# Kernel tuning notes

Measured on AMD Instinct MI355X. Metric: run time of the kernel, lower is better.

Reference implementation:

```python
import jax, jax.numpy as jnp
import numpy as np
import math

B, T, NC = 16, 256, 2
_NS = (9, 9, 11, 11, 9, 20)  # legacy6 region node counts
_OUT, _RF, _FD, _NH, _FF = 32, 64, 128, 4, 2048


def _region_adj(n):
    # chain + second-order edges (legacy6), plus self-loops; GCN sym-normalized
    A = np.zeros((n, n), np.float32)
    for i in range(n - 1):
        A[i, i + 1] = A[i + 1, i] = 1.0
    for i in range(n - 2):
        A[i, i + 2] = A[i + 2, i] = 1.0
    A = A + np.eye(n, dtype=np.float32)
    d = A.sum(1) ** -0.5
    return jnp.asarray(d[:, None] * A * d[None, :])

_ADJS = [_region_adj(n) for n in _NS]


def _pe_table(t, d):
    pos = np.arange(t, dtype=np.float32)[:, None]
    div = np.exp(np.arange(0, d, 2, dtype=np.float32) * (-math.log(10000.0) / d))
    pe = np.zeros((t, d), np.float32)
    pe[:, 0::2] = np.sin(pos * div)
    pe[:, 1::2] = np.cos(pos * div)
    return jnp.asarray(pe)

_PE = _pe_table(T, _FD)


def _ln(x, g, b, eps=1e-5):
    m = jnp.mean(x, -1, keepdims=True)
    v = jnp.mean((x - m) ** 2, -1, keepdims=True)
    return (x - m) / jnp.sqrt(v + eps) * g + b


def _mha(q, kv, qkv_w, qkv_b, ow, ob, nh):
    d = q.shape[-1]
    hd = d // nh
    wq, wk, wv = jnp.split(qkv_w, 3, axis=1)
    bq, bk, bv = jnp.split(qkv_b, 3)
    def sp(x):
        return x.reshape(x.shape[0], x.shape[1], nh, hd).transpose(0, 2, 1, 3)
    Q, K, V = sp(q @ wq + bq), sp(kv @ wk + bk), sp(kv @ wv + bv)
    att = jax.nn.softmax(jnp.einsum('bhqd,bhkd->bhqk', Q, K) / jnp.sqrt(jnp.float32(hd)), axis=-1)
    o = jnp.einsum('bhqk,bhkd->bhqd', att, V).transpose(0, 2, 1, 3).reshape(q.shape[0], q.shape[1], d)
    return o @ ow + ob


def _tel(x, qkv_w, qkv_b, ow, ob, l1g, l1b, f1w, f1b, f2w, f2b, l2g, l2b, nh):
    # torch post-norm TransformerEncoderLayer (relu FFN, eval mode: no dropout)
    x = _ln(x + _mha(x, x, qkv_w, qkv_b, ow, ob, nh), l1g, l1b)
    ff = jax.nn.relu(x @ f1w + f1b) @ f2w + f2b
    return _ln(x + ff, l2g, l2b)


def setup_inputs() -> dict:
    key = jax.random.key(0)
    ks = iter(jax.random.split(key, 80))
    def nrm(shape, s=0.05):
        return jax.random.normal(next(ks), shape, jnp.float32) * s
    inp = {}
    for name, n in zip(('x_ljaw', 'x_rjaw', 'x_leye', 'x_reye', 'x_nose', 'x_mouth'), _NS):
        inp[name] = jax.random.normal(next(ks), (B, T, n, 11), jnp.float32)
    inp['global_feats'] = jax.random.normal(next(ks), (B, T, 4), jnp.float32)
    inp['global_alpha'] = jnp.float32(0.2)
    inp['gcn1_w'] = nrm((6, 11, _OUT)); inp['gcn1_b'] = jnp.zeros((6, _OUT))
    inp['gcn2_w'] = nrm((6, _OUT, _OUT)); inp['gcn2_b'] = jnp.zeros((6, _OUT))
    inp['rln_g'] = jnp.ones((6, _RF)); inp['rln_b'] = jnp.zeros((6, _RF))
    inp['sp_qkv_w'] = nrm((_RF, 3 * _RF)); inp['sp_qkv_b'] = jnp.zeros((3 * _RF,))
    inp['sp_out_w'] = nrm((_RF, _RF)); inp['sp_out_b'] = jnp.zeros((_RF,))
    inp['sp_ln1_g'] = jnp.ones((_RF,)); inp['sp_ln1_b'] = jnp.zeros((_RF,))
    inp['sp_ff1_w'] = nrm((_RF, _FF)); inp['sp_ff1_b'] = jnp.zeros((_FF,))
    inp['sp_ff2_w'] = nrm((_FF, _RF)); inp['sp_ff2_b'] = jnp.zeros((_RF,))
    inp['sp_ln2_g'] = jnp.ones((_RF,)); inp['sp_ln2_b'] = jnp.zeros((_RF,))
    priors = np.array([0.3, 0.3, 0.8, 0.8, 0.4, 1.0], np.float32)
    inp['region_logits'] = jnp.asarray(np.log(np.expm1(priors)).reshape(1, 6, 1))
    inp['gate1_w'] = nrm((_RF, 32)); inp['gate1_b'] = jnp.zeros((32,))
    inp['gate2_w'] = nrm((32, 1)); inp['gate2_b'] = jnp.zeros((1,))
    inp['ca_qkv_w'] = nrm((_RF, 3 * _RF)); inp['ca_qkv_b'] = jnp.zeros((3 * _RF,))
    inp['ca_out_w'] = nrm((_RF, _RF)); inp['ca_out_b'] = jnp.zeros((_RF,))
    inp['ca_ln_g'] = jnp.ones((_RF,)); inp['ca_ln_b'] = jnp.zeros((_RF,))
    inp['glob_w'] = nrm((4, _RF)); inp['glob_b'] = jnp.zeros((_RF,))
    inp['glob_ln_g'] = jnp.ones((_RF,)); inp['glob_ln_b'] = jnp.zeros((_RF,))
    inp['fused_ln_g'] = jnp.ones((_FD,)); inp['fused_ln_b'] = jnp.zeros((_FD,))
    inp['tp_qkv_w'] = nrm((_FD, 3 * _FD)); inp['tp_qkv_b'] = jnp.zeros((3 * _FD,))
    inp['tp_out_w'] = nrm((_FD, _FD)); inp['tp_out_b'] = jnp.zeros((_FD,))
    inp['tp_ln1_g'] = jnp.ones((_FD,)); inp['tp_ln1_b'] = jnp.zeros((_FD,))
    inp['tp_ff1_w'] = nrm((_FD, _FF)); inp['tp_ff1_b'] = jnp.zeros((_FF,))
    inp['tp_ff2_w'] = nrm((_FF, _FD)); inp['tp_ff2_b'] = jnp.zeros((_FD,))
    inp['tp_ln2_g'] = jnp.ones((_FD,)); inp['tp_ln2_b'] = jnp.zeros((_FD,))
    inp['attnproj_w'] = nrm((_FD, 1)); inp['attnproj_b'] = jnp.zeros((1,))
    inp['cls1_w'] = nrm((_FD, _OUT)); inp['cls1_b'] = jnp.zeros((_OUT,))
    inp['cls_ln_g'] = jnp.ones((_OUT,)); inp['cls_ln_b'] = jnp.zeros((_OUT,))
    inp['cls2_w'] = nrm((_OUT, NC)); inp['cls2_b'] = jnp.zeros((NC,))
    return inp


def reference(x_ljaw, x_rjaw, x_leye, x_reye, x_nose, x_mouth, global_feats, global_alpha, gcn1_w, gcn1_b, gcn2_w, gcn2_b, rln_g, rln_b, sp_qkv_w, sp_qkv_b, sp_out_w, sp_out_b, sp_ln1_g, sp_ln1_b, sp_ff1_w, sp_ff1_b, sp_ff2_w, sp_ff2_b, sp_ln2_g, sp_ln2_b, region_logits, gate1_w, gate1_b, gate2_w, gate2_b, ca_qkv_w, ca_qkv_b, ca_out_w, ca_out_b, ca_ln_g, ca_ln_b, glob_w, glob_b, glob_ln_g, glob_ln_b, fused_ln_g, fused_ln_b, tp_qkv_w, tp_qkv_b, tp_out_w, tp_out_b, tp_ln1_g, tp_ln1_b, tp_ff1_w, tp_ff1_b, tp_ff2_w, tp_ff2_b, tp_ln2_g, tp_ln2_b, attnproj_w, attnproj_b, cls1_w, cls1_b, cls_ln_g, cls_ln_b, cls2_w, cls2_b):
    xs = (x_ljaw, x_rjaw, x_leye, x_reye, x_nose, x_mouth)
    Bc, Tc = x_ljaw.shape[0], x_ljaw.shape[1]
    # per-region 2-layer GCN + concat(mean,max) node pooling -> (B,T,64) tokens
    toks = []
    for i in range(6):
        A = _ADJS[i]
        h = jax.nn.relu(jnp.einsum('nm,btmf->btnf', A, xs[i] @ gcn1_w[i]) + gcn1_b[i])
        h = jax.nn.relu(jnp.einsum('nm,btmf->btnf', A, h @ gcn2_w[i]) + gcn2_b[i])
        feat = jnp.concatenate([h.mean(2), h.max(2)], -1)
        toks.append(_ln(feat, rln_g[i], rln_b[i]))
    tok = jnp.stack(toks, 2).reshape(Bc * Tc, 6, _RF)
    # spatial transformer over the 6 region tokens per frame
    tok = _tel(tok, sp_qkv_w, sp_qkv_b, sp_out_w, sp_out_b, sp_ln1_g, sp_ln1_b, sp_ff1_w, sp_ff1_b, sp_ff2_w, sp_ff2_b, sp_ln2_g, sp_ln2_b, _NH)
    # learned region priors (softplus) * per-sample sigmoid gates
    rw = jax.nn.softplus(region_logits)
    gate = jax.nn.sigmoid(jax.nn.relu(tok @ gate1_w + gate1_b) @ gate2_w + gate2_b)
    tok = tok * rw * gate
    # cross-attn fusion: mean-region query attends over region tokens
    q = jnp.mean(tok, 1, keepdims=True)
    attn = _mha(q, tok, ca_qkv_w, ca_qkv_b, ca_out_w, ca_out_b, _NH)
    fused_r = _ln(q[:, 0] + attn[:, 0], ca_ln_g, ca_ln_b)
    # gated global branch (4 -> 64), concat to fused_dim=128
    g = jax.nn.relu(_ln(global_feats.reshape(Bc * Tc, 4) @ glob_w + glob_b, glob_ln_g, glob_ln_b))
    g = jnp.tanh(global_alpha) * g
    fused = _ln(jnp.concatenate([fused_r, g], -1), fused_ln_g, fused_ln_b).reshape(Bc, Tc, _FD)
    # temporal transformer + attention pooling over time
    fused = fused + _PE[None, :Tc]
    h = _tel(fused, tp_qkv_w, tp_qkv_b, tp_out_w, tp_out_b, tp_ln1_g, tp_ln1_b, tp_ff1_w, tp_ff1_b, tp_ff2_w, tp_ff2_b, tp_ln2_g, tp_ln2_b, _NH)
    wt = jax.nn.softmax(h @ attnproj_w + attnproj_b, axis=1)
    pooled = jnp.sum(wt * h, 1)
    z = jax.nn.relu(_ln(pooled @ cls1_w + cls1_b, cls_ln_g, cls_ln_b))
    return z @ cls2_w + cls2_b
```

## Files before the change

kernel.cpp:

```cpp
#include <hip/hip_runtime.h>
#include <math.h>
#include <stddef.h>

#define NFRM 4096
#define NBATCH 16

typedef __attribute__((ext_vector_type(8))) short short8v;
typedef __attribute__((ext_vector_type(4))) float f32x4;
#define MFMA_BF16(a,b,c) __builtin_amdgcn_mfma_f32_16x16x32_bf16(a,b,c,0,0,0)

__device__ inline float wsum64(float v){
  #pragma unroll
  for(int m=32;m>=1;m>>=1) v += __shfl_xor(v, m, 64);
  return v;
}

__device__ inline float pe_val(int t,int d){
  int k = d >> 1;
  float div = expf(-(float)(2*k) * (9.210340371976184f/128.f));
  float ang = (float)t * div;
  return (d & 1) ? cosf(ang) : sinf(ang);
}

__device__ inline void bf16split(float x, unsigned short &h, unsigned short &l){
  unsigned u = __float_as_uint(x);
  unsigned r = (u + 0x7FFFu + ((u>>16)&1u)) & 0xFFFF0000u;
  h = (unsigned short)(r>>16);
  float rem = x - __uint_as_float(r);
  unsigned u2 = __float_as_uint(rem);
  unsigned r2 = (u2 + 0x7FFFu + ((u2>>16)&1u));
  l = (unsigned short)(r2>>16);
}

__global__ __launch_bounds__(64) void pack_w_kernel(
    const float* __restrict__ w, unsigned short* __restrict__ hi,
    unsigned short* __restrict__ lo, int K, int N)
{
  int ntile = blockIdx.x, s = blockIdx.y, lane = threadIdx.x;
  int n = ntile*16 + (lane & 15);
  int k0 = s*32 + (lane>>4)*8;
  size_t off = (((size_t)ntile*(K/32) + s)*64 + lane)*8;
  #pragma unroll
  for(int e=0;e<8;e++){
    float v = w[(size_t)(k0+e)*N + n];
    unsigned short h,l;
    bf16split(v,h,l);
    hi[off+e]=h; lo[off+e]=l;
  }
}

template<int D, int NS>
__global__ __launch_bounds__(256) void ffn_mfma_partial(
    const float* __restrict__ X, float* __restrict__ P,
    const unsigned short* __restrict__ w1h, const unsigned short* __restrict__ w1l,
    const float* __restrict__ b1,
    const unsigned short* __restrict__ w2h, const unsigned short* __restrict__ w2l)
{
  constexpr int TM=32, JC=128;
  constexpr int KS1 = D/32;
  constexpr int NT2W = (D/16)/4;
  constexpr int HS = 2048/NS;
  constexpr int NCH = HS/JC;
  constexpr int HP = JC + 8;
  __shared__ unsigned short Hh[TM][HP];
  __shared__ unsigned short Hl[TM][HP];
  int tid = threadIdx.x;
  int lane = tid & 63, w = tid >> 6;
  int ar = lane & 15, ak = lane >> 4;
  size_t Ntok = (size_t)gridDim.x*TM;
  const float* Xb = X + (size_t)blockIdx.x*TM*D;

  short8v xah[2][KS1], xal[2][KS1];
  #pragma unroll
  for(int mt=0;mt<2;mt++){
    #pragma unroll
    for(int s=0;s<KS1;s++){
      const float* xp = Xb + (size_t)(mt*16+ar)*D + s*32 + ak*8;
      #pragma unroll
      for(int e=0;e<8;e++){
        unsigned short h,l;
        bf16split(xp[e],h,l);
        xah[mt][s][e]=(short)h; xal[mt][s][e]=(short)l;
      }
    }
  }

  f32x4 acc2[2][NT2W];
  #pragma unroll
  for(int mt=0;mt<2;mt++)
    #pragma unroll
    for(int nt=0;nt<NT2W;nt++)
      acc2[mt][nt] = (f32x4){0.f,0.f,0.f,0.f};

  for(int ch=0; ch<NCH; ch++){
    int jc = blockIdx.y*HS + ch*JC;
    f32x4 a1[2][2];
    #pragma unroll
    for(int mt=0;mt<2;mt++){ a1[mt][0]=(f32x4){0,0,0,0}; a1[mt][1]=(f32x4){0,0,0,0}; }
    #pragma unroll
    for(int s=0;s<KS1;s++){
      #pragma unroll
      for(int nt=0;nt<2;nt++){
        int ntile1 = (jc + w*32 + nt*16) >> 4;
        size_t off = (((size_t)ntile1*KS1 + s)*64 + lane)*8;
        short8v bh = *(const short8v*)(w1h + off);
        short8v bl = *(const short8v*)(w1l + off);
        #pragma unroll
        for(int mt=0;mt<2;mt++){
          a1[mt][nt] = MFMA_BF16(xah[mt][s], bh, a1[mt][nt]);
          a1[mt][nt] = MFMA_BF16(xah[mt][s], bl, a1[mt][nt]);
          a1[mt][nt] = MFMA_BF16(xal[mt][s], bh, a1[mt][nt]);
        }
      }
    }
    __syncthreads();
    #pragma unroll
    for(int nt=0;nt<2;nt++){
      int colBase = w*32 + nt*16 + ar;
      float bval = b1[jc + colBase];
      #pragma unroll
      for(int mt=0;mt<2;mt++){
        #pragma unroll
        for(int r=0;r<4;r++){
          float hv = a1[mt][nt][r] + bval;
          hv = fmaxf(hv, 0.f);
          unsigned short h,l;
          bf16split(hv,h,l);
          int row = mt*16 + ak*4 + r;
          Hh[row][colBase]=h; Hl[row][colBase]=l;
        }
      }
    }
    __syncthreads();
    #pragma unroll
    for(int s2=0;s2<4;s2++){
      short8v ah[2], al[2];
      #pragma unroll
      for(int mt=0;mt<2;mt++){
        ah[mt] = *(const short8v*)&Hh[mt*16+ar][s2*32 + ak*8];
        al[mt] = *(const short8v*)&Hl[mt*16+ar][s2*32 + ak*8];
      }
      #pragma unroll
      for(int nt=0;nt<NT2W;nt++){
        int ntile2 = w*NT2W + nt;
        int kstep2 = (jc >> 5) + s2;
        size_t off = (((size_t)ntile2*64 + kstep2)*64 + lane)*8;
        short8v bh = *(const short8v*)(w2h + off);
        short8v bl = *(const short8v*)(w2l + off);
        #pragma unroll
        for(int mt=0;mt<2;mt++){
          acc2[mt][nt] = MFMA_BF16(ah[mt], bh, acc2[mt][nt]);
          acc2[mt][nt] = MFMA_BF16(ah[mt], bl, acc2[mt][nt]);
          acc2[mt][nt] = MFMA_BF16(al[mt], bh, acc2[mt][nt]);
        }
      }
    }
  }
  float* Pb = P + (size_t)blockIdx.y*Ntok*D + (size_t)blockIdx.x*TM*D;
  #pragma unroll
  for(int mt=0;mt<2;mt++){
    #pragma unroll
    for(int nt=0;nt<NT2W;nt++){
      int col = (w*NT2W + nt)*16 + ar;
      #pragma unroll
      for(int r=0;r<4;r++){
        int row = mt*16 + ak*4 + r;
        Pb[(size_t)row*D + col] = acc2[mt][nt][r];
      }
    }
  }
}

template<int D, int NS>
__global__ __launch_bounds__(256) void ffn_combine_kernel(
    const float* __restrict__ X, const float* __restrict__ P,
    float* __restrict__ Y,
    const float* __restrict__ b2,
    const float* __restrict__ lg, const float* __restrict__ lb)
{
  constexpr int EPL = D/64;
  int tid=threadIdx.x;
  int lane = tid & 63;
  size_t Ntok = (size_t)gridDim.x*4;
  size_t row = (size_t)blockIdx.x*4 + (tid>>6);
  size_t base = row*D;
  float e[EPL];
  float s=0.f;
  #pragma unroll
  for(int i=0;i<EPL;i++){
    int c = i*64+lane;
    float v = X[base+c] + b2[c];
    #pragma unroll
    for(int sp=0;sp<NS;sp++) v += P[(size_t)sp*Ntok*D + base + c];
    e[i]=v; s+=v;
  }
  float mm = wsum64(s)*(1.f/D);
  float s2=0.f;
  #pragma unroll
  for(int i=0;i<EPL;i++){ float d=e[i]-mm; s2+=d*d; }
  float rs = rsqrtf(wsum64(s2)*(1.f/D)+1e-5f);
  #pragma unroll
  for(int i=0;i<EPL;i++){
    int c=i*64+lane;
    Y[base+c] = (e[i]-mm)*rs*lg[c]+lb[c];
  }
}

__global__ __launch_bounds__(256) void gcn_kernel(
    const float* __restrict__ x0,const float* __restrict__ x1,
    const float* __restrict__ x2,const float* __restrict__ x3,
    const float* __restrict__ x4,const float* __restrict__ x5,
    const float* __restrict__ g1w,const float* __restrict__ g1b,
    const float* __restrict__ g2w,const float* __restrict__ g2b,
    const float* __restrict__ rg,const float* __restrict__ rb,
    float* __restrict__ tok)
{
  int tid=threadIdx.x;
  int lane = tid & 63, w = tid >> 6;
  int f = blockIdx.x*4 + w;
  int r = blockIdx.y;
  int n = (r==5) ? 20 : ((r==2 || r==3) ? 11 : 9);
  const float* xr = (r==0)?x0:(r==1)?x1:(r==2)?x2:(r==3)?x3:(r==4)?x4:x5;

  __shared__ float xs[4][220];
  __shared__ float t0g[4][768];
  __shared__ float t1[4][640];
  __shared__ float C[20][5];
  __shared__ float W1s[11*32];
  __shared__ float W2s[32*32];
  __shared__ float b1s[32], b2s[32];

  for(int i=tid;i<4*768;i+=256) ((float*)t0g)[i]=0.f;
  for(int i=tid;i<352;i+=256) W1s[i]=g1w[r*11*32+i];
  for(int i=tid;i<1024;i+=256) W2s[i]=g2w[r*32*32+i];
  if(tid<32){ b1s[tid]=g1b[r*32+tid]; b2s[tid]=g2b[r*32+tid]; }
  if(tid<100){
    int node=tid/5, j=tid%5, m=node+j-2;
    float cf=0.f;
    if(node<n && m>=0 && m<n){
      int di = 1 + min(node,2) + min(n-1-node,2);
      int dm = 1 + min(m,2) + min(n-1-m,2);
      cf = rsqrtf((float)(di*dm));
    }
    C[node][j]=cf;
  }
  for(int i=lane;i<n*11;i+=64) xs[w][i] = xr[(size_t)f*n*11 + i];
  __syncthreads();
  for(int i=lane;i<n*32;i+=64){
    int node=i>>5, c=i&31;
    float s=0.f;
    #pragma unroll
    for(int k=0;k<11;k++) s += xs[w][node*11+k]*W1s[k*32+c];
    t0g[w][(node+2)*32+c]=s;
  }
  __syncthreads();
  for(int i=lane;i<n*32;i+=64){
    int node=i>>5, c=i&31;
    float s=b1s[c];
    #pragma unroll
    for(int j=0;j<5;j++) s += C[node][j]*t0g[w][(node+j)*32+c];
    t1[w][i]=fmaxf(s,0.f);
  }
  __syncthreads();
  for(int i=lane;i<n*32;i+=64){
    int node=i>>5, c=i&31;
    float s=0.f;
    #pragma unroll
    for(int k=0;k<32;k++) s += t1[w][node*32+k]*W2s[k*32+c];
    t0g[w][(node+2)*32+c]=s;
  }
  __syncthreads();
  for(int i=lane;i<n*32;i+=64){
    int node=i>>5, c=i&31;
    float s=b2s[c];
    #pragma unroll
    for(int j=0;j<5;j++) s += C[node][j]*t0g[w][(node+j)*32+c];
    t1[w][i]=fmaxf(s,0.f);
  }
  __syncthreads();
  float v;
  if(lane<32){
    float s=0.f;
    for(int m=0;m<n;m++) s += t1[w][m*32+lane];
    v = s/(float)n;
  } else {
    int c=lane-32;
    float mx=-1e30f;
    for(int m=0;m<n;m++) mx = fmaxf(mx, t1[w][m*32+c]);
    v = mx;
  }
  float m1 = wsum64(v)*(1.f/64.f);
  float d1 = v - m1;
  float var = wsum64(d1*d1)*(1.f/64.f);
  float y = d1*rsqrtf(var+1e-5f)*rg[r*64+lane] + rb[r*64+lane];
  tok[((size_t)f*6+r)*64+lane] = y;
}

__global__ __launch_bounds__(256) void sp_attn_kernel(
    float* __restrict__ tok,
    const float* __restrict__ qkvw,const float* __restrict__ qkvb,
    const float* __restrict__ ow,const float* __restrict__ ob,
    const float* __restrict__ l1g,const float* __restrict__ l1b)
{
  __shared__ float Xs[24][64];
  __shared__ float QKV[24][192];
  __shared__ float SC[4][144];
  __shared__ float AO[24][64];
  int tid=threadIdx.x;
  int f0 = blockIdx.x*4;
  float* Xf = &Xs[0][0];
  for(int i=tid;i<1536;i+=256) Xf[i] = tok[(size_t)f0*384 + i];
  __syncthreads();
  {
    int cg = tid & 31, c0 = cg*6;
    int rg = tid >> 5, r0 = rg*3;
    float acc[3][6];
    #pragma unroll
    for(int m=0;m<3;m++)
      #pragma unroll
      for(int j=0;j<6;j++) acc[m][j]=qkvb[c0+j];
    for(int k=0;k<64;k++){
      float wv[6];
      #pragma unroll
      for(int j=0;j<6;j++) wv[j]=qkvw[k*192+c0+j];
      float xv0=Xs[r0][k], xv1=Xs[r0+1][k], xv2=Xs[r0+2][k];
      #pragma unroll
      for(int j=0;j<6;j++){
        acc[0][j]+=xv0*wv[j];
        acc[1][j]+=xv1*wv[j];
        acc[2][j]+=xv2*wv[j];
      }
    }
    #pragma unroll
    for(int m=0;m<3;m++)
      #pragma unroll
      for(int j=0;j<6;j++) QKV[r0+m][c0+j]=acc[m][j];
  }
  __syncthreads();
  for(int i=tid;i<576;i+=256){
    int fr=i/144, rest=i%144;
    int h=rest/36, qi=(rest%36)/6, ki=rest%6;
    float s=0.f;
    #pragma unroll
    for(int d=0;d<16;d++) s += QKV[fr*6+qi][h*16+d]*QKV[fr*6+ki][64+h*16+d];
    SC[fr][rest]=s*0.25f;
  }
  __syncthreads();
  if(tid<96){
    int fr=tid/24, idx=tid%24;
    int base=idx*6;
    float mx=-1e30f;
    for(int k=0;k<6;k++) mx=fmaxf(mx,SC[fr][base+k]);
    float sm=0.f;
    for(int k=0;k<6;k++){ float e=expf(SC[fr][base+k]-mx); SC[fr][base+k]=e; sm+=e; }
    float rr=1.f/sm;
    for(int k=0;k<6;k++) SC[fr][base+k]*=rr;
  }
  __syncthreads();
  for(int i=tid;i<1536;i+=256){
    int fr=i/384, rem=i%384;
    int row=rem/64, c=rem&63, h=c/16;
    float s=0.f;
    #pragma unroll
    for(int k=0;k<6;k++) s += SC[fr][h*36+row*6+k]*QKV[fr*6+k][128+c];
    AO[fr*6+row][c]=s;
  }
  __syncthreads();
  {
    int cg = tid & 31, c0 = cg*2;
    int rg = tid >> 5, r0 = rg*3;
    float acc[3][2];
    #pragma unroll
    for(int m=0;m<3;m++){ acc[m][0]=ob[c0]; acc[m][1]=ob[c0+1]; }
    for(int k=0;k<64;k++){
      float w0=ow[k*64+c0], w1=ow[k*64+c0+1];
      float a0=AO[r0][k], a1=AO[r0+1][k], a2=AO[r0+2][k];
      acc[0][0]+=a0*w0; acc[0][1]+=a0*w1;
      acc[1][0]+=a1*w0; acc[1][1]+=a1*w1;
      acc[2][0]+=a2*w0; acc[2][1]+=a2*w1;
    }
    #pragma unroll
    for(int m=0;m<3;m++){
      QKV[r0+m][c0]   = Xs[r0+m][c0]   + acc[m][0];
      QKV[r0+m][c0+1] = Xs[r0+m][c0+1] + acc[m][1];
    }
  }
  __syncthreads();
  {
    int lane = tid & 63, w = tid >> 6;
    #pragma unroll
    for(int rr=0;rr<6;rr++){
      int row = w*6+rr;
      float v=QKV[row][lane];
      float mm=wsum64(v)*(1.f/64.f);
      float d=v-mm;
      float var=wsum64(d*d)*(1.f/64.f);
      tok[(size_t)f0*384 + row*64 + lane]=d*rsqrtf(var+1e-5f)*l1g[lane]+l1b[lane];
    }
  }
}

template<int D, int TM>
__global__ __launch_bounds__(256) void ffn_ln_kernel(
    const float* __restrict__ X, float* __restrict__ Yout,
    const float* __restrict__ w1,const float* __restrict__ b1,
    const float* __restrict__ w2,const float* __restrict__ b2,
    const float* __restrict__ lg,const float* __restrict__ lb)
{
  constexpr int JC = 128;
  constexpr int JS = JC + 4;
  constexpr int M1 = TM/8;
  constexpr int CG = D/4;
  constexpr int MG2 = 256/CG;
  constexpr int M2 = TM/MG2;
  __shared__ float Xs[TM*D];
  __shared__ float Hs[TM*JS];
  int tid=threadIdx.x;
  const float* Xb = X + (size_t)blockIdx.x*TM*D;
  for(int i=tid;i<TM*D;i+=256) Xs[i]=Xb[i];

  int jg = tid & 31, j0 = jg*4;
  int mg1 = tid >> 5;
  int m10 = mg1*M1;
  int cg = tid % CG, c0 = cg*4;
  int mg2 = tid / CG;
  int m20 = mg2*M2;

  float acc[M2][4];
  #pragma unroll
  for(int m=0;m<M2;m++){ acc[m][0]=0.f;acc[m][1]=0.f;acc[m][2]=0.f;acc[m][3]=0.f; }

  __syncthreads();
  for(int jc=0;jc<2048;jc+=JC){
    float a1[M1][4];
    float4 bv = *(const float4*)&b1[jc+j0];
    #pragma unroll
    for(int m=0;m<M1;m++){ a1[m][0]=bv.x;a1[m][1]=bv.y;a1[m][2]=bv.z;a1[m][3]=bv.w; }
    for(int k0=0;k0<D;k0+=4){
      float4 wr0 = *(const float4*)&w1[(size_t)(k0+0)*2048 + jc + j0];
      float4 wr1 = *(const float4*)&w1[(size_t)(k0+1)*2048 + jc + j0];
      float4 wr2 = *(const float4*)&w1[(size_t)(k0+2)*2048 + jc + j0];
      float4 wr3 = *(const float4*)&w1[(size_t)(k0+3)*2048 + jc + j0];
      #pragma unroll
      for(int m=0;m<M1;m++){
        float4 xv = *(const float4*)&Xs[(m10+m)*D + k0];
        a1[m][0] += xv.x*wr0.x + xv.y*wr1.x + xv.z*wr2.x + xv.w*wr3.x;
        a1[m][1] += xv.x*wr0.y + xv.y*wr1.y + xv.z*wr2.y + xv.w*wr3.y;
        a1[m][2] += xv.x*wr0.z + xv.y*wr1.z + xv.z*wr2.z + xv.w*wr3.z;
        a1[m][3] += xv.x*wr0.w + xv.y*wr1.w + xv.z*wr2.w + xv.w*wr3.w;
      }
    }
    #pragma unroll
    for(int m=0;m<M1;m++){
      float4 hv;
      hv.x=fmaxf(a1[m][0],0.f); hv.y=fmaxf(a1[m][1],0.f);
      hv.z=fmaxf(a1[m][2],0.f); hv.w=fmaxf(a1[m][3],0.f);
      *(float4*)&Hs[(m10+m)*JS + j0] = hv;
    }
    __syncthreads();
    for(int jj0=0;jj0<JC;jj0+=4){
      float4 w20 = *(const float4*)&w2[(size_t)(jc+jj0+0)*D + c0];
      float4 w21 = *(const float4*)&w2[(size_t)(jc+jj0+1)*D + c0];
      float4 w22 = *(const float4*)&w2[(size_t)(jc+jj0+2)*D + c0];
      float4 w23 = *(const float4*)&w2[(size_t)(jc+jj0+3)*D + c0];
      #pragma unroll
      for(int m=0;m<M2;m++){
        float4 hv = *(const float4*)&Hs[(m20+m)*JS + jj0];
        acc[m][0] += hv.x*w20.x + hv.y*w21.x + hv.z*w22.x + hv.w*w23.x;
        acc[m][1] += hv.x*w20.y + hv.y*w21.y + hv.z*w22.y + hv.w*w23.y;
        acc[m][2] += hv.x*w20.z + hv.y*w21.z + hv.z*w22.z + hv.w*w23.z;
        acc[m][3] += hv.x*w20.w + hv.y*w21.w + hv.z*w22.w + hv.w*w23.w;
      }
    }
    __syncthreads();
  }
  {
    float4 b2v = *(const float4*)&b2[c0];
    #pragma unroll
    for(int m=0;m<M2;m++){
      int row = m20+m;
      float4 xv = *(const float4*)&Xs[row*D + c0];
      float4 yv;
      yv.x = xv.x + acc[m][0] + b2v.x;
      yv.y = xv.y + acc[m][1] + b2v.y;
      yv.z = xv.z + acc[m][2] + b2v.z;
      yv.w = xv.w + acc[m][3] + b2v.w;
      *(float4*)&Hs[row*D + c0] = yv;
    }
  }
  __syncthreads();
  constexpr int EPL = D/64;
  int lane = tid & 63, wv = tid >> 6;
  float* Yb = Yout + (size_t)blockIdx.x*TM*D;
  for(int row=wv; row<TM; row+=4){
    float e[EPL];
    float s=0.f;
    #pragma unroll
    for(int i=0;i<EPL;i++){ e[i]=Hs[row*D + i*64 + lane]; s+=e[i]; }
    float mm = wsum64(s)*(1.f/D);
    float s2=0.f;
    #pragma unroll
    for(int i=0;i<EPL;i++){ float d=e[i]-mm; s2+=d*d; }
    float rs = rsqrtf(wsum64(s2)*(1.f/D)+1e-5f);
    #pragma unroll
    for(int i=0;i<EPL;i++)
      Yb[row*D + i*64 + lane] = (e[i]-mm)*rs*lg[i*64+lane]+lb[i*64+lane];
  }
}

__global__ __launch_bounds__(256) void fuse_kernel(
    const float* __restrict__ tok, const float* __restrict__ gfeat,
    const float* __restrict__ alpha_p, const float* __restrict__ rlogit,
    const float* __restrict__ g1w,const float* __restrict__ g1b,
    const float* __restrict__ g2w,const float* __restrict__ g2b,
    const float* __restrict__ caqw,const float* __restrict__ caqb,
    const float* __restrict__ caow,const float* __restrict__ caob,
    const float* __restrict__ calng,const float* __restrict__ calnb,
    const float* __restrict__ gw,const float* __restrict__ gb,
    const float* __restrict__ glng,const float* __restrict__ glnb,
    const float* __restrict__ flng,const float* __restrict__ flnb,
    float* __restrict__ fused)
{
  int tid=threadIdx.x;
  int lane = tid & 63, w = tid >> 6;
  int f = blockIdx.x*4 + w;
  __shared__ float X[4][384];
  __shared__ float G1[4][192];
  __shared__ float gt[4][6];
  __shared__ float qv[4][64];
  __shared__ float Qs[4][64];
  __shared__ float KK[4][384], VV[4][384];
  __shared__ float sc[4][24];
  __shared__ float AOs[4][64];

  const float* trow = tok + (size_t)f*384;
  for(int i=lane;i<384;i+=64) X[w][i]=trow[i];
  __syncthreads();
  for(int i=lane;i<192;i+=64){
    int rr=i/32, j=i%32;
    float s=g1b[j];
    #pragma unroll
    for(int k=0;k<64;k++) s += X[w][rr*64+k]*g1w[k*32+j];
    G1[w][i]=fmaxf(s,0.f);
  }
  __syncthreads();
  if(lane<6){
    float s=g2b[0];
    #pragma unroll
    for(int k=0;k<32;k++) s += G1[w][lane*32+k]*g2w[k];
    float gate = 1.f/(1.f+expf(-s));
    float rw = log1pf(expf(rlogit[lane]));
    gt[w][lane]=gate*rw;
  }
  __syncthreads();
  for(int i=lane;i<384;i+=64) X[w][i]*=gt[w][i/64];
  __syncthreads();
  {
    float s=0.f;
    #pragma unroll
    for(int rr=0;rr<6;rr++) s+=X[w][rr*64+lane];
    qv[w][lane]=s*(1.f/6.f);
  }
  __syncthreads();
  {
    float s=caqb[lane];
    #pragma unroll
    for(int k=0;k<64;k++) s += qv[w][k]*caqw[k*192+lane];
    Qs[w][lane]=s;
  }
  for(int i=lane;i<384;i+=64){
    int rr=i/64, c=i%64;
    float sk=caqb[64+c], sv=caqb[128+c];
    #pragma unroll
    for(int k=0;k<64;k++){
      float xv=X[w][rr*64+k];
      sk += xv*caqw[k*192+64+c];
      sv += xv*caqw[k*192+128+c];
    }
    KK[w][i]=sk; VV[w][i]=sv;
  }
  __syncthreads();
  if(lane<24){
    int h=lane/6, ki=lane%6;
    float s=0.f;
    #pragma unroll
    for(int d=0;d<16;d++) s += Qs[w][h*16+d]*KK[w][ki*64+h*16+d];
    sc[w][lane]=s*0.25f;
  }
  __syncthreads();
  if(lane<4){
    float mx=-1e30f;
    for(int k=0;k<6;k++) mx=fmaxf(mx,sc[w][lane*6+k]);
    float sm=0.f;
    for(int k=0;k<6;k++){ float e=expf(sc[w][lane*6+k]-mx); sc[w][lane*6+k]=e; sm+=e; }
    float rr=1.f/sm;
    for(int k=0;k<6;k++) sc[w][lane*6+k]*=rr;
  }
  __syncthreads();
  {
    int h=lane/16;
    float s=0.f;
    #pragma unroll
    for(int k=0;k<6;k++) s += sc[w][h*6+k]*VV[w][k*64+lane];
    AOs[w][lane]=s;
  }
  __syncthreads();
  float pr;
  {
    float s=caob[lane];
    #pragma unroll
    for(int k=0;k<64;k++) s += AOs[w][k]*caow[k*64+lane];
    pr = qv[w][lane] + s;
  }
  float m1=wsum64(pr)*(1.f/64.f);
  float d1=pr-m1;
  float v1=wsum64(d1*d1)*(1.f/64.f);
  float fr = d1*rsqrtf(v1+1e-5f)*calng[lane]+calnb[lane];
  float gvv;
  {
    float s=gb[lane];
    #pragma unroll
    for(int k=0;k<4;k++) s += gfeat[(size_t)f*4+k]*gw[k*64+lane];
    gvv=s;
  }
  float m2=wsum64(gvv)*(1.f/64.f);
  float d2=gvv-m2;
  float v2=wsum64(d2*d2)*(1.f/64.f);
  float gg = fmaxf(d2*rsqrtf(v2+1e-5f)*glng[lane]+glnb[lane],0.f)*tanhf(alpha_p[0]);
  float sm_ = wsum64(fr+gg)*(1.f/128.f);
  float da=fr-sm_, db=gg-sm_;
  float vv = wsum64(da*da+db*db)*(1.f/128.f);
  float rs = rsqrtf(vv+1e-5f);
  int t = f & 255;
  fused[(size_t)f*128+lane]     = da*rs*flng[lane]+flnb[lane]         + pe_val(t,lane);
  fused[(size_t)f*128+64+lane]  = db*rs*flng[64+lane]+flnb[64+lane]   + pe_val(t,64+lane);
}

__global__ __launch_bounds__(256) void tqkv_gemm_kernel(
    const float* __restrict__ X, float* __restrict__ Y,
    const float* __restrict__ w, const float* __restrict__ b)
{
  __shared__ float Xs[32*128];
  int tid=threadIdx.x;
  const float* Xb = X + (size_t)blockIdx.x*32*128;
  for(int i=tid;i<4096;i+=256) Xs[i]=Xb[i];
  __syncthreads();
  int cg = tid & 31, c0 = cg*4;
  int mg = tid >> 5, m0 = mg*4;
  float* Yb = Y + (size_t)blockIdx.x*32*384;
  int oc = blockIdx.y*128;
  float acc[4][4];
  float4 bv = *(const float4*)&b[oc+c0];
  #pragma unroll
  for(int m=0;m<4;m++){ acc[m][0]=bv.x;acc[m][1]=bv.y;acc[m][2]=bv.z;acc[m][3]=bv.w; }
  for(int k0=0;k0<128;k0+=4){
    float4 w0 = *(const float4*)&w[(k0+0)*384 + oc + c0];
    float4 w1 = *(const float4*)&w[(k0+1)*384 + oc + c0];
    float4 w2 = *(const float4*)&w[(k0+2)*384 + oc + c0];
    float4 w3 = *(const float4*)&w[(k0+3)*384 + oc + c0];
    #pragma unroll
    for(int m=0;m<4;m++){
      float4 xv = *(const float4*)&Xs[(m0+m)*128 + k0];
      acc[m][0] += xv.x*w0.x + xv.y*w1.x + xv.z*w2.x + xv.w*w3.x;
      acc[m][1] += xv.x*w0.y + xv.y*w1.y + xv.z*w2.y + xv.w*w3.y;
      acc[m][2] += xv.x*w0.z + xv.y*w1.z + xv.z*w2.z + xv.w*w3.z;
      acc[m][3] += xv.x*w0.w + xv.y*w1.w + xv.z*w2.w + xv.w*w3.w;
    }
  }
  #pragma unroll
  for(int m=0;m<4;m++){
    float4 yv; yv.x=acc[m][0];yv.y=acc[m][1];yv.z=acc[m][2];yv.w=acc[m][3];
    *(float4*)&Yb[(m0+m)*384 + oc + c0] = yv;
  }
}

__global__ __launch_bounds__(256) void tattn_split_kernel(
    const float* __restrict__ qkv, float* __restrict__ PO,
    float* __restrict__ PM, float* __restrict__ PL)
{
  int b=blockIdx.x, h=blockIdx.y, s=blockIdx.z, tid=threadIdx.x;
  __shared__ float Ksh[32*32];
  __shared__ float Vsh[32*32];
  const float* base = qkv + (size_t)b*256*384;
  int k0 = s*32;
  for(int i=tid;i<1024;i+=256){
    int t=i>>5, d=i&31;
    Ksh[i]=base[(size_t)(k0+t)*384+128+h*32+d];
    Vsh[i]=base[(size_t)(k0+t)*384+256+h*32+d];
  }
  float q[32];
  #pragma unroll
  for(int d=0;d<32;d++) q[d]=base[(size_t)tid*384+h*32+d];
  __syncthreads();
  const float scale=0.17677669529663687f;
  float sc[32];
  float mx=-1e30f;
  #pragma unroll
  for(int k=0;k<32;k++){
    float sv=0.f;
    #pragma unroll
    for(int d=0;d<32;d++) sv += q[d]*Ksh[k*32+d];
    sc[k]=sv*scale;
    mx=fmaxf(mx,sc[k]);
  }
  float l=0.f, o[32];
  #pragma unroll
  for(int d=0;d<32;d++) o[d]=0.f;
  #pragma unroll
  for(int k=0;k<32;k++){
    float p=expf(sc[k]-mx);
    l+=p;
    #pragma unroll
    for(int d=0;d<32;d++) o[d]+=p*Vsh[k*32+d];
  }
  int bh = b*4+h;
  size_t idx = ((size_t)s*64 + bh)*256 + tid;
  PM[idx]=mx; PL[idx]=l;
  float* po = PO + idx*32;
  #pragma unroll
  for(int d=0;d<32;d++) po[d]=o[d];
}

__global__ __launch_bounds__(256) void attn_combine_kernel(
    const float* __restrict__ PO, const float* __restrict__ PM,
    const float* __restrict__ PL, float* __restrict__ obuf)
{
  int tid=threadIdx.x;
  int ql = tid>>5, d = tid&31;
  int bh = blockIdx.x >> 5;
  int qc = blockIdx.x & 31;
  int q = qc*8 + ql;
  float ms[8], ls[8];
  float M=-1e30f;
  #pragma unroll
  for(int s=0;s<8;s++){
    size_t idx = ((size_t)s*64 + bh)*256 + q;
    ms[s]=PM[idx]; ls[s]=PL[idx];
    M=fmaxf(M,ms[s]);
  }
  float L=0.f, ov=0.f;
  #pragma unroll
  for(int s=0;s<8;s++){
    float w = expf(ms[s]-M);
    L += ls[s]*w;
    size_t idx = ((size_t)s*64 + bh)*256 + q;
    ov += w * PO[idx*32 + d];
  }
  int b = bh>>2, h = bh&3;
  obuf[(size_t)(b*256+q)*128 + h*32 + d] = ov / L;
}

__global__ __launch_bounds__(256) void tattn_kernel(
    const float* __restrict__ qkv, float* __restrict__ obuf)
{
  int b=blockIdx.x, h=blockIdx.y, tid=threadIdx.x;
  __shared__ float Ksh[256*32];
  __shared__ float Vsh[64*32];
  const float* base = qkv + (size_t)b*256*384;
  for(int i=tid;i<8192;i+=256){
    int t=i>>5, d=i&31;
    Ksh[i]=base[t*384+128+h*32+d];
  }
  float q[32];
  #pragma unroll
  for(int d=0;d<32;d++) q[d]=base[(size_t)tid*384+h*32+d];
  __syncthreads();
  const float scale=0.17677669529663687f;
  float mx=-1e30f;
  for(int k=0;k<256;k++){
    float s=0.f;
    #pragma unroll
    for(int d=0;d<32;d++) s += q[d]*Ksh[k*32+d];
    mx=fmaxf(mx,s*scale);
  }
  float l=0.f, o[32];
  #pragma unroll
  for(int d=0;d<32;d++) o[d]=0.f;
  for(int kc=0;kc<256;kc+=64){
    __syncthreads();
    for(int i=tid;i<2048;i+=256){
      int t=i>>5, d=i&31;
      Vsh[i]=base[(size_t)(kc+t)*384+256+h*32+d];
    }
    __syncthreads();
    for(int k2=0;k2<64;k2++){
      float s=0.f;
      #pragma unroll
      for(int d=0;d<32;d++) s += q[d]*Ksh[(kc+k2)*32+d];
      float p=expf(s*scale-mx);
      l+=p;
      #pragma unroll
      for(int d=0;d<32;d++) o[d]+=p*Vsh[k2*32+d];
    }
  }
  float inv=1.f/l;
  float* orow = obuf + (size_t)(b*256+tid)*128 + h*32;
  #pragma unroll
  for(int d=0;d<32;d++) orow[d]=o[d]*inv;
}

__global__ __launch_bounds__(256) void tproj_gemm_kernel(
    const float* __restrict__ O, float* __restrict__ F,
    const float* __restrict__ w, const float* __restrict__ b,
    const float* __restrict__ lg, const float* __restrict__ lb)
{
  __shared__ float Os[32*128];
  __shared__ float Ys[32*128];
  int tid=threadIdx.x;
  const float* Ob = O + (size_t)blockIdx.x*32*128;
  float* Fb = F + (size_t)blockIdx.x*32*128;
  for(int i=tid;i<4096;i+=256) Os[i]=Ob[i];
  __syncthreads();
  int cg = tid & 31, c0 = cg*4;
  int mg = tid >> 5, m0 = mg*4;
  float acc[4][4];
  float4 bv = *(const float4*)&b[c0];
  #pragma unroll
  for(int m=0;m<4;m++){ acc[m][0]=bv.x;acc[m][1]=bv.y;acc[m][2]=bv.z;acc[m][3]=bv.w; }
  for(int k0=0;k0<128;k0+=4){
    float4 w0 = *(const float4*)&w[(k0+0)*128 + c0];
    float4 w1 = *(const float4*)&w[(k0+1)*128 + c0];
    float4 w2 = *(const float4*)&w[(k0+2)*128 + c0];
    float4 w3 = *(const float4*)&w[(k0+3)*128 + c0];
    #pragma unroll
    for(int m=0;m<4;m++){
      float4 xv = *(const float4*)&Os[(m0+m)*128 + k0];
      acc[m][0] += xv.x*w0.x + xv.y*w1.x + xv.z*w2.x + xv.w*w3.x;
      acc[m][1] += xv.x*w0.y + xv.y*w1.y + xv.z*w2.y + xv.w*w3.y;
      acc[m][2] += xv.x*w0.z + xv.y*w1.z + xv.z*w2.z + xv.w*w3.z;
      acc[m][3] += xv.x*w0.w + xv.y*w1.w + xv.z*w2.w + xv.w*w3.w;
    }
  }
  #pragma unroll
  for(int m=0;m<4;m++){
    float4 fv = *(const float4*)&Fb[(m0+m)*128 + c0];
    float4 yv;
    yv.x = fv.x + acc[m][0]; yv.y = fv.y + acc[m][1];
    yv.z = fv.z + acc[m][2]; yv.w = fv.w + acc[m][3];
    *(float4*)&Ys[(m0+m)*128 + c0] = yv;
  }
  __syncthreads();
  int lane = tid & 63, wv = tid >> 6;
  for(int row=wv; row<32; row+=4){
    float e0=Ys[row*128+lane], e1=Ys[row*128+64+lane];
    float mm = wsum64(e0+e1)*(1.f/128.f);
    float d0=e0-mm, d1=e1-mm;
    float rs = rsqrtf(wsum64(d0*d0+d1*d1)*(1.f/128.f)+1e-5f);
    Fb[row*128+lane]    = d0*rs*lg[lane]+lb[lane];
    Fb[row*128+64+lane] = d1*rs*lg[64+lane]+lb[64+lane];
  }
}

__global__ __launch_bounds__(256) void pool_cls_kernel(
    const float* __restrict__ h2,
    const float* __restrict__ apw,const float* __restrict__ apb,
    const float* __restrict__ c1w,const float* __restrict__ c1b,
    const float* __restrict__ clng,const float* __restrict__ clnb,
    const float* __restrict__ c2w,const float* __restrict__ c2b,
    float* __restrict__ out)
{
  int b=blockIdx.x, tid=threadIdx.x;
  __shared__ float lg[256];
  __shared__ float wt[256];
  __shared__ float invs[1];
  __shared__ float pooled[128];
  __shared__ float z[32];
  const float* H = h2 + (size_t)b*256*128;
  {
    float s=apb[0];
    #pragma unroll
    for(int k=0;k<128;k++) s += H[(size_t)tid*128+k]*apw[k];
    lg[tid]=s;
  }
  __syncthreads();
  if(tid==0){
    float mx=-1e30f;
    for(int i=0;i<256;i++) mx=fmaxf(mx,lg[i]);
    float sm=0.f;
    for(int i=0;i<256;i++){ float e=expf(lg[i]-mx); wt[i]=e; sm+=e; }
    invs[0]=1.f/sm;
  }
  __syncthreads();
  float inv=invs[0];
  if(tid<128){
    float s=0.f;
    for(int t=0;t<256;t++) s += wt[t]*inv*H[(size_t)t*128+tid];
    pooled[tid]=s;
  }
  __syncthreads();
  if(tid<32){
    float s=c1b[tid];
    #pragma unroll
    for(int k=0;k<128;k++) s += pooled[k]*c1w[k*32+tid];
    z[tid]=s;
  }
  __syncthreads();
  if(tid==0){
    float m=0.f;
    for(int i=0;i<32;i++) m+=z[i];
    m *= (1.f/32.f);
    float v=0.f;
    for(int i=0;i<32;i++){ float d=z[i]-m; v+=d*d; }
    v *= (1.f/32.f);
    float rs=rsqrtf(v+1e-5f);
    for(int i=0;i<32;i++) z[i]=fmaxf((z[i]-m)*rs*clng[i]+clnb[i],0.f);
  }
  __syncthreads();
  if(tid<2){
    float s=c2b[tid];
    #pragma unroll
    for(int k=0;k<32;k++) s += z[k]*c2w[k*2+tid];
    out[b*2+tid]=s;
  }
}

extern "C" void kernel_launch(void* const* d_in, const int* in_sizes, int n_in,
                              void* d_out, int out_size, void* d_ws, size_t ws_size,
                              hipStream_t stream) {
  const float* x0 = (const float*)d_in[0];
  const float* x1 = (const float*)d_in[1];
  const float* x2 = (const float*)d_in[2];
  const float* x3 = (const float*)d_in[3];
  const float* x4 = (const float*)d_in[4];
  const float* x5 = (const float*)d_in[5];
  const float* gfeat   = (const float*)d_in[6];
  const float* alpha_p = (const float*)d_in[7];
  const float* g1w = (const float*)d_in[8];
  const float* g1b = (const float*)d_in[9];
  const float* g2w = (const float*)d_in[10];
  const float* g2b = (const float*)d_in[11];
  const float* rlg = (const float*)d_in[12];
  const float* rlb = (const float*)d_in[13];
  const float* spqkvw = (const float*)d_in[14];
  const float* spqkvb = (const float*)d_in[15];
  const float* spow = (const float*)d_in[16];
  const float* spob = (const float*)d_in[17];
  const float* spl1g = (const float*)d_in[18];
  const float* spl1b = (const float*)d_in[19];
  const float* spf1w = (const float*)d_in[20];
  const float* spf1b = (const float*)d_in[21];
  const float* spf2w = (const float*)d_in[22];
  const float* spf2b = (const float*)d_in[23];
  const float* spl2g = (const float*)d_in[24];
  const float* spl2b = (const float*)d_in[25];
  const float* rlogit = (const float*)d_in[26];
  const float* gate1w = (const float*)d_in[27];
  const float* gate1b = (const float*)d_in[28];
  const float* gate2w = (const float*)d_in[29];
  const float* gate2b = (const float*)d_in[30];
  const float* caqkvw = (const float*)d_in[31];
  const float* caqkvb = (const float*)d_in[32];
  const float* caow = (const float*)d_in[33];
  const float* caob = (const float*)d_in[34];
  const float* calng = (const float*)d_in[35];
  const float* calnb = (const float*)d_in[36];
  const float* globw = (const float*)d_in[37];
  const float* globb = (const float*)d_in[38];
  const float* glng = (const float*)d_in[39];
  const float* glnb = (const float*)d_in[40];
  const float* flng = (const float*)d_in[41];
  const float* flnb = (const float*)d_in[42];
  const float* tpqkvw = (const float*)d_in[43];
  const float* tpqkvb = (const float*)d_in[44];
  const float* tpow = (const float*)d_in[45];
  const float* tpob = (const float*)d_in[46];
  const float* tpl1g = (const float*)d_in[47];
  const float* tpl1b = (const float*)d_in[48];
  const float* tpf1w = (const float*)d_in[49];
  const float* tpf1b = (const float*)d_in[50];
  const float* tpf2w = (const float*)d_in[51];
  const float* tpf2b = (const float*)d_in[52];
  const float* tpl2g = (const float*)d_in[53];
  const float* tpl2b = (const float*)d_in[54];
  const float* apw = (const float*)d_in[55];
  const float* apb = (const float*)d_in[56];
  const float* c1w = (const float*)d_in[57];
  const float* c1b = (const float*)d_in[58];
  const float* clng = (const float*)d_in[59];
  const float* clnb = (const float*)d_in[60];
  const float* c2w = (const float*)d_in[61];
  const float* c2b = (const float*)d_in[62];

  float* ws = (float*)d_ws;
  float* tok   = ws;
  float* fused = tok   + (size_t)NFRM*384;
  float* qkv   = fused + (size_t)NFRM*128;
  float* obuf  = qkv   + (size_t)NFRM*384;
  float* part  = obuf  + (size_t)NFRM*128;
  size_t part_elems = (size_t)2*24576*64;
  unsigned short* pk = (unsigned short*)(part + part_elems);
  unsigned short* sp1h = pk;
  unsigned short* sp1l = sp1h + 131072;
  unsigned short* sp2h = sp1l + 131072;
  unsigned short* sp2l = sp2h + 131072;
  unsigned short* tp1h = sp2l + 131072;
  unsigned short* tp1l = tp1h + 262144;
  unsigned short* tp2h = tp1l + 262144;
  unsigned short* tp2l = tp2h + 262144;
  size_t pack_ushorts = 4*131072 + 4*262144;
  size_t need = ((size_t)NFRM*384 + NFRM*128 + NFRM*384 + NFRM*128 + part_elems)*4
              + pack_ushorts*2;
  bool mfma_ok = (ws_size >= need);

  float* attnPO = (float*)(pk + pack_ushorts);
  float* attnPM = attnPO + (size_t)8*64*256*32;
  float* attnPL = attnPM + (size_t)8*64*256;
  size_t need2 = need + ((size_t)8*64*256*32 + 2*(size_t)8*64*256)*4;
  bool attn_ok = (ws_size >= need2);

  if(mfma_ok){
    pack_w_kernel<<<dim3(128,2),64,0,stream>>>(spf1w, sp1h, sp1l, 64, 2048);
    pack_w_kernel<<<dim3(4,64),64,0,stream>>>(spf2w, sp2h, sp2l, 2048, 64);
    pack_w_kernel<<<dim3(128,4),64,0,stream>>>(tpf1w, tp1h, tp1l, 128, 2048);
    pack_w_kernel<<<dim3(8,64),64,0,stream>>>(tpf2w, tp2h, tp2l, 2048, 128);
  }

  gcn_kernel<<<dim3(NFRM/4,6),256,0,stream>>>(x0,x1,x2,x3,x4,x5,g1w,g1b,g2w,g2b,rlg,rlb,tok);
  sp_attn_kernel<<<NFRM/4,256,0,stream>>>(tok,spqkvw,spqkvb,spow,spob,spl1g,spl1b);
  if(mfma_ok){
    ffn_mfma_partial<64,2><<<dim3(768,2),256,0,stream>>>(tok,part,sp1h,sp1l,spf1b,sp2h,sp2l);
    ffn_combine_kernel<64,2><<<24576/4,256,0,stream>>>(tok,part,tok,spf2b,spl2g,spl2b);
  } else {
    ffn_ln_kernel<64,32><<<768,256,0,stream>>>(tok,tok,spf1w,spf1b,spf2w,spf2b,spl2g,spl2b);
  }
  fuse_kernel<<<NFRM/4,256,0,stream>>>(tok,gfeat,alpha_p,rlogit,gate1w,gate1b,gate2w,gate2b,
                                    caqkvw,caqkvb,caow,caob,calng,calnb,
                                    globw,globb,glng,glnb,flng,flnb,fused);
  tqkv_gemm_kernel<<<dim3(128,3),256,0,stream>>>(fused,qkv,tpqkvw,tpqkvb);
  if(attn_ok){
    tattn_split_kernel<<<dim3(NBATCH,4,8),256,0,stream>>>(qkv,attnPO,attnPM,attnPL);
    attn_combine_kernel<<<64*32,256,0,stream>>>(attnPO,attnPM,attnPL,obuf);
  } else {
    tattn_kernel<<<dim3(NBATCH,4),256,0,stream>>>(qkv,obuf);
  }
  tproj_gemm_kernel<<<128,256,0,stream>>>(obuf,fused,tpow,tpob,tpl1g,tpl1b);
  if(mfma_ok){
    ffn_mfma_partial<128,4><<<dim3(128,4),256,0,stream>>>(fused,part,tp1h,tp1l,tpf1b,tp2h,tp2l);
    ffn_combine_kernel<128,4><<<NFRM/4,256,0,stream>>>(fused,part,obuf,tpf2b,tpl2g,tpl2b);
  } else {
    ffn_ln_kernel<128,16><<<256,256,0,stream>>>(fused,obuf,tpf1w,tpf1b,tpf2w,tpf2b,tpl2g,tpl2b);
  }
  pool_cls_kernel<<<NBATCH,256,0,stream>>>(obuf,apw,apb,c1w,c1b,clng,clnb,c2w,c2b,(float*)d_out);
}
```

Measured before the change: 353.3 us.

## Merge weight-pack launches and restructure GCN kernel with register-held weights

Result: faster. 334.9 us (-5.2%).

```diff
diff --git a/kernel.cpp b/kernel.cpp
--- a/kernel.cpp
+++ b/kernel.cpp
@@ -32,11 +32,20 @@
   l = (unsigned short)(r2>>16);
 }
 
-__global__ __launch_bounds__(64) void pack_w_kernel(
-    const float* __restrict__ w, unsigned short* __restrict__ hi,
-    unsigned short* __restrict__ lo, int K, int N)
-{
-  int ntile = blockIdx.x, s = blockIdx.y, lane = threadIdx.x;
+__global__ __launch_bounds__(64) void pack_all_kernel(
+    const float* __restrict__ spf1w, const float* __restrict__ spf2w,
+    const float* __restrict__ tpf1w, const float* __restrict__ tpf2w,
+    unsigned short* __restrict__ sp1h, unsigned short* __restrict__ sp1l,
+    unsigned short* __restrict__ sp2h, unsigned short* __restrict__ sp2l,
+    unsigned short* __restrict__ tp1h, unsigned short* __restrict__ tp1l,
+    unsigned short* __restrict__ tp2h, unsigned short* __restrict__ tp2l)
+{
+  int b = blockIdx.x, lane = threadIdx.x;
+  const float* w; unsigned short *hi, *lo; int K, N, ntile, s;
+  if(b < 256){        w=spf1w; hi=sp1h; lo=sp1l; K=64;   N=2048; ntile=b&127;        s=b>>7; }
+  else if(b < 512){   int bb=b-256;  w=spf2w; hi=sp2h; lo=sp2l; K=2048; N=64;   ntile=bb&3;   s=bb>>2; }
+  else if(b < 1024){  int bb=b-512;  w=tpf1w; hi=tp1h; lo=tp1l; K=128;  N=2048; ntile=bb&127; s=bb>>7; }
+  else {              int bb=b-1024; w=tpf2w; hi=tp2h; lo=tp2l; K=2048; N=128;  ntile=bb&7;   s=bb>>3; }
   int n = ntile*16 + (lane & 15);
   int k0 = s*32 + (lane>>4)*8;
   size_t off = (((size_t)ntile*(K/32) + s)*64 + lane)*8;
@@ -206,7 +215,7 @@
   }
 }
 
-__global__ __launch_bounds__(256) void gcn_kernel(
+__global__ __launch_bounds__(128) void gcn_kernel(
     const float* __restrict__ x0,const float* __restrict__ x1,
     const float* __restrict__ x2,const float* __restrict__ x3,
     const float* __restrict__ x4,const float* __restrict__ x5,
@@ -217,23 +226,24 @@
 {
   int tid=threadIdx.x;
   int lane = tid & 63, w = tid >> 6;
-  int f = blockIdx.x*4 + w;
+  int f = blockIdx.x*2 + w;
   int r = blockIdx.y;
   int n = (r==5) ? 20 : ((r==2 || r==3) ? 11 : 9);
   const float* xr = (r==0)?x0:(r==1)?x1:(r==2)?x2:(r==3)?x3:(r==4)?x4:x5;
-
-  __shared__ float xs[4][220];
-  __shared__ float t0g[4][768];
-  __shared__ float t1[4][640];
+  int c = lane & 31;
+
+  __shared__ float xs[2][20*12];
+  __shared__ float t0g[2][24*32];
+  __shared__ float t1s[2][20*32];
   __shared__ float C[20][5];
-  __shared__ float W1s[11*32];
-  __shared__ float W2s[32*32];
-  __shared__ float b1s[32], b2s[32];
-
-  for(int i=tid;i<4*768;i+=256) ((float*)t0g)[i]=0.f;
-  for(int i=tid;i<352;i+=256) W1s[i]=g1w[r*11*32+i];
-  for(int i=tid;i<1024;i+=256) W2s[i]=g2w[r*32*32+i];
-  if(tid<32){ b1s[tid]=g1b[r*32+tid]; b2s[tid]=g2b[r*32+tid]; }
+
+  float W1c[11], W2c[32];
+  #pragma unroll
+  for(int k=0;k<11;k++) W1c[k]=g1w[r*352 + k*32 + c];
+  #pragma unroll
+  for(int k=0;k<32;k++) W2c[k]=g2w[r*1024 + k*32 + c];
+  float b1c = g1b[r*32+c], b2c = g2b[r*32+c];
+
   if(tid<100){
     int node=tid/5, j=tid%5, m=node+j-2;
     float cf=0.f;
@@ -244,49 +254,62 @@
     }
     C[node][j]=cf;
   }
-  for(int i=lane;i<n*11;i+=64) xs[w][i] = xr[(size_t)f*n*11 + i];
+  for(int i=lane;i<128;i+=64){
+    int row4=i>>5, col=i&31;
+    int row = (row4<2) ? row4 : (n+row4);
+    t0g[w][row*32+col]=0.f;
+  }
+  for(int i=lane;i<n*12;i+=64){
+    int node=i/12, k=i-node*12;
+    xs[w][i] = (k<11) ? xr[(size_t)f*n*11 + node*11 + k] : 0.f;
+  }
   __syncthreads();
   for(int i=lane;i<n*32;i+=64){
-    int node=i>>5, c=i&31;
+    int node=i>>5;
+    float4 xa = *(const float4*)&xs[w][node*12];
+    float4 xb = *(const float4*)&xs[w][node*12+4];
+    float4 xc = *(const float4*)&xs[w][node*12+8];
+    float s = xa.x*W1c[0]+xa.y*W1c[1]+xa.z*W1c[2]+xa.w*W1c[3]
+            + xb.x*W1c[4]+xb.y*W1c[5]+xb.z*W1c[6]+xb.w*W1c[7]
+            + xc.x*W1c[8]+xc.y*W1c[9]+xc.z*W1c[10];
+    t0g[w][(node+2)*32+c]=s;
+  }
+  __syncthreads();
+  for(int i=lane;i<n*32;i+=64){
+    int node=i>>5;
+    float s=b1c;
+    #pragma unroll
+    for(int j=0;j<5;j++) s += C[node][j]*t0g[w][(node+j)*32+c];
+    t1s[w][i]=fmaxf(s,0.f);
+  }
+  __syncthreads();
+  for(int i=lane;i<n*32;i+=64){
+    int node=i>>5;
     float s=0.f;
     #pragma unroll
-    for(int k=0;k<11;k++) s += xs[w][node*11+k]*W1s[k*32+c];
+    for(int k0=0;k0<32;k0+=4){
+      float4 tv = *(const float4*)&t1s[w][node*32+k0];
+      s += tv.x*W2c[k0] + tv.y*W2c[k0+1] + tv.z*W2c[k0+2] + tv.w*W2c[k0+3];
+    }
     t0g[w][(node+2)*32+c]=s;
   }
   __syncthreads();
   for(int i=lane;i<n*32;i+=64){
-    int node=i>>5, c=i&31;
-    float s=b1s[c];
+    int node=i>>5;
+    float s=b2c;
     #pragma unroll
     for(int j=0;j<5;j++) s += C[node][j]*t0g[w][(node+j)*32+c];
-    t1[w][i]=fmaxf(s,0.f);
-  }
-  __syncthreads();
-  for(int i=lane;i<n*32;i+=64){
-    int node=i>>5, c=i&31;
-    float s=0.f;
-    #pragma unroll
-    for(int k=0;k<32;k++) s += t1[w][node*32+k]*W2s[k*32+c];
-    t0g[w][(node+2)*32+c]=s;
-  }
-  __syncthreads();
-  for(int i=lane;i<n*32;i+=64){
-    int node=i>>5, c=i&31;
-    float s=b2s[c];
-    #pragma unroll
-    for(int j=0;j<5;j++) s += C[node][j]*t0g[w][(node+j)*32+c];
-    t1[w][i]=fmaxf(s,0.f);
+    t1s[w][i]=fmaxf(s,0.f);
   }
   __syncthreads();
   float v;
   if(lane<32){
     float s=0.f;
-    for(int m=0;m<n;m++) s += t1[w][m*32+lane];
+    for(int m=0;m<n;m++) s += t1s[w][m*32+lane];
     v = s/(float)n;
   } else {
-    int c=lane-32;
     float mx=-1e30f;
-    for(int m=0;m<n;m++) mx = fmaxf(mx, t1[w][m*32+c]);
+    for(int m=0;m<n;m++) mx = fmaxf(mx, t1s[w][m*32+c]);
     v = mx;
   }
   float m1 = wsum64(v)*(1.f/64.f);
@@ -1009,13 +1032,11 @@
   bool attn_ok = (ws_size >= need2);
 
   if(mfma_ok){
-    pack_w_kernel<<<dim3(128,2),64,0,stream>>>(spf1w, sp1h, sp1l, 64, 2048);
-    pack_w_kernel<<<dim3(4,64),64,0,stream>>>(spf2w, sp2h, sp2l, 2048, 64);
-    pack_w_kernel<<<dim3(128,4),64,0,stream>>>(tpf1w, tp1h, tp1l, 128, 2048);
-    pack_w_kernel<<<dim3(8,64),64,0,stream>>>(tpf2w, tp2h, tp2l, 2048, 128);
-  }
-
-  gcn_kernel<<<dim3(NFRM/4,6),256,0,stream>>>(x0,x1,x2,x3,x4,x5,g1w,g1b,g2w,g2b,rlg,rlb,tok);
+    pack_all_kernel<<<1536,64,0,stream>>>(spf1w,spf2w,tpf1w,tpf2w,
+                                          sp1h,sp1l,sp2h,sp2l,tp1h,tp1l,tp2h,tp2l);
+  }
+
+  gcn_kernel<<<dim3(NFRM/2,6),128,0,stream>>>(x0,x1,x2,x3,x4,x5,g1w,g1b,g2w,g2b,rlg,rlb,tok);
   sp_attn_kernel<<<NFRM/4,256,0,stream>>>(tok,spqkvw,spqkvb,spow,spob,spl1g,spl1b);
   if(mfma_ok){
     ffn_mfma_partial<64,2><<<dim3(768,2),256,0,stream>>>(tok,part,sp1h,sp1l,spf1b,sp2h,sp2l);
```
